# Performance work log

Measured on AMD Instinct MI355X. Metric: run time of the kernel, lower is better.

Reference implementation:

```python
import jax, jax.numpy as jnp
import numpy as np

OBJ_DIM, REL_DIM, EFF_DIM = 5, 1, 100
REL_HID, OBJ_HID, OUT_DIM = 150, 100, 2


def _init_linear(key, fan_in, fan_out):
    kw, kb = jax.random.split(key)
    bound = 1.0 / np.sqrt(fan_in)
    W = jax.random.uniform(kw, (fan_in, fan_out), jnp.float32, -bound, bound)
    b = jax.random.uniform(kb, (fan_out,), jnp.float32, -bound, bound)
    return W, b


def setup_inputs() -> dict:
    key = jax.random.key(0)
    ks = jax.random.split(key, 12)
    B, N, R = 64, 100, 9900
    inp = {
        "objects": jax.random.normal(ks[0], (B, N, OBJ_DIM), jnp.float32),
        "sender_relations": jax.random.uniform(ks[1], (B, N, R), jnp.float32),
        "receiver_relations": jax.random.uniform(ks[2], (B, N, R), jnp.float32),
        "relation_info": jax.random.normal(ks[3], (B, R, REL_DIM), jnp.float32),
    }
    # relational MLP: (2*obj + rel) -> 150 -> 150 -> effect_dim, ReLU after each
    rW1, rb1 = _init_linear(ks[4], 2 * OBJ_DIM + REL_DIM, REL_HID)
    rW2, rb2 = _init_linear(ks[5], REL_HID, REL_HID)
    rW3, rb3 = _init_linear(ks[6], REL_HID, EFF_DIM)
    # object MLP: (obj + effect) -> 100 -> 100 -> 2
    oW1, ob1 = _init_linear(ks[7], OBJ_DIM + EFF_DIM, OBJ_HID)
    oW2, ob2 = _init_linear(ks[8], OBJ_HID, OBJ_HID)
    oW3, ob3 = _init_linear(ks[9], OBJ_HID, OUT_DIM)
    inp.update(rW1=rW1, rb1=rb1, rW2=rW2, rb2=rb2, rW3=rW3, rb3=rb3,
               oW1=oW1, ob1=ob1, oW2=oW2, ob2=ob2, oW3=oW3, ob3=ob3)
    return inp


def _relational_mlp(x, rW1, rb1, rW2, rb2, rW3, rb3):
    h = jax.nn.relu(x @ rW1 + rb1)
    h = jax.nn.relu(h @ rW2 + rb2)
    return jax.nn.relu(h @ rW3 + rb3)


def _object_mlp(x, oW1, ob1, oW2, ob2, oW3, ob3):
    h = jax.nn.relu(x @ oW1 + ob1)
    h = jax.nn.relu(h @ oW2 + ob2)
    return h @ oW3 + ob3


def reference(objects, sender_relations, receiver_relations, relation_info,
              rW1, rb1, rW2, rb2, rW3, rb3, oW1, ob1, oW2, ob2, oW3, ob3):
    # gather: [B,R,N] @ [B,N,D] -> [B,R,D]
    senders = jnp.einsum('bnr,bnd->brd', sender_relations, objects)
    receivers = jnp.einsum('bnr,bnd->brd', receiver_relations, objects)
    rel_in = jnp.concatenate([senders, receivers, relation_info], axis=2)
    effects = _relational_mlp(rel_in, rW1, rb1, rW2, rb2, rW3, rb3)  # [B,R,E]
    # scatter: [B,N,R] @ [B,R,E] -> [B,N,E]
    effect_receivers = jnp.einsum('bnr,bre->bne', receiver_relations, effects)
    obj_in = jnp.concatenate([objects, effect_receivers], axis=2)
    return _object_mlp(obj_in, oW1, ob1, oW2, ob2, oW3, ob3)  # [B,N,2]
```

## Files before the change

kernel.cpp:

```cpp
#include <hip/hip_runtime.h>
#include <hip/hip_bf16.h>

#define B_    64
#define N_    100
#define R_    9900
#define OBJD  5
#define EFF   100

typedef __bf16 bf16x8 __attribute__((ext_vector_type(8)));
typedef __bf16 bf16x2 __attribute__((ext_vector_type(2)));
typedef short  short8v __attribute__((ext_vector_type(8)));
typedef float  f32x4  __attribute__((ext_vector_type(4)));

__device__ __forceinline__ ushort f2bf(float f) {
    __bf16 h = (__bf16)f;
    return __builtin_bit_cast(ushort, h);
}
__device__ __forceinline__ unsigned pk2(float a, float b) {
    bf16x2 v; v[0] = (__bf16)a; v[1] = (__bf16)b;
    return __builtin_bit_cast(unsigned, v);
}
__device__ __forceinline__ float bf2f(ushort u) {
    union { unsigned u; float f; } x; x.u = ((unsigned)u) << 16;
    return x.f;
}

#define WTR_OBJ 52096

__global__ __launch_bounds__(256) void k_prepw(
    const float* __restrict__ W1, const float* __restrict__ W2,
    const float* __restrict__ W3, const float* __restrict__ O1,
    const float* __restrict__ O2, const float* __restrict__ O3,
    ushort* __restrict__ WTR)
{
    const int img = blockIdx.x;
    if (img == 0) {
        for (int idx = threadIdx.x; idx < 6400; idx += 256) {
            const int c = idx / 40, k = idx - (idx/40)*40;
            WTR[idx] = f2bf((c < 150 && k < 11) ? W1[k*150 + c] : 0.f);
        }
    } else if (img == 1) {
        for (int idx = threadIdx.x; idx < 26880; idx += 256) {
            const int c = idx / 168, k = idx - (idx/168)*168;
            WTR[6400 + idx] = f2bf((c < 150 && k < 150) ? W2[k*150 + c] : 0.f);
        }
    } else if (img == 2) {
        for (int idx = threadIdx.x; idx < 18816; idx += 256) {
            const int c = idx / 168, k = idx - (idx/168)*168;
            WTR[33280 + idx] = f2bf((c < 100 && k < 150) ? W3[k*100 + c] : 0.f);
        }
    } else {
        const int j = img - 3;
        ushort* dst = WTR + WTR_OBJ + (size_t)j*11520;
        for (int idx = threadIdx.x; idx < 11520; idx += 256) {
            const int cc = idx / 72, kk = idx - (idx/72)*72;
            float v = 0.f;
            if (kk < 64) {
                if (j < 4) {
                    const int kg = j*64 + kk;
                    int row = -1;
                    if (kg < 5) row = kg;
                    else if (kg >= 8 && kg < 108) row = kg - 3;
                    else if (kg >= 108 && kg < 208) row = kg - 103;
                    if (cc < 100 && row >= 0) v = O1[row*100 + cc];
                } else if (j < 6) {
                    const int kg = (j-4)*64 + kk;
                    if (cc < 100 && kg < 100) v = O2[kg*100 + cc];
                } else {
                    const int kg = (j-6)*64 + kk;
                    if (cc < 2 && kg < 100) v = O3[kg*2 + cc];
                }
            }
            dst[idx] = f2bf(v);
        }
    }
}

#define LW1 0
#define LW2 6400
#define LW3 33280
#define LBA 52096
#define LBB 60160
#define LACT 68224
#define LBIAS 78976
#define LGB  79776
#define LTOT 81312

__global__ __launch_bounds__(512, 1) void k_relmlp_p(
    const float* __restrict__ obj, const float* __restrict__ SR,
    const float* __restrict__ RR, const float* __restrict__ RI,
    const ushort* __restrict__ WTR,
    const float* __restrict__ b1, const float* __restrict__ b2,
    const float* __restrict__ b3, float* __restrict__ ER)
{
    __shared__ __align__(16) ushort lds[LTOT];
    const int t  = threadIdx.x;
    const int b  = blockIdx.x >> 2;
    const int qt = blockIdx.x & 3;
    const int lane = t & 63, w = t >> 6;
    const int lo = lane & 15, hi = lane >> 4;
    const int mt = w & 3, nh = w >> 2;
    const int q  = t & 7,  rr = t >> 3;

    #pragma unroll
    for (int j = 0; j < 13; ++j) {
        const int idx = t + j*512;
        if (idx < 6512)
            reinterpret_cast<uint4*>(lds)[idx] =
                reinterpret_cast<const uint4*>(WTR)[idx];
    }
    {
        float* bias_w = (float*)(lds + LBIAS);
        if (t < 150)      bias_w[t] = b1[t];
        else if (t < 300) bias_w[t] = b2[t-150];
        else if (t < 400) bias_w[t] = b3[t-300];
    }
    if (t < 216) {
        ushort* base = lds + ((t < 108) ? LBA : LBB) + 100*72;
        const int k = (t < 108) ? t : t - 108;
        *reinterpret_cast<uint4*>(base + k*8) = make_uint4(0u, 0u, 0u, 0u);
    }
    if (t < 64) {
        ushort* gb0 = lds + LGB + t*24;
        gb0[11] = 0;
        *reinterpret_cast<ushort4*>(&gb0[12]) = make_ushort4(0,0,0,0);
        *reinterpret_cast<ushort4*>(&gb0[16]) = make_ushort4(0,0,0,0);
        *reinterpret_cast<ushort4*>(&gb0[20]) = make_ushort4(0,0,0,0);
    }

    float objv[13][5];
    {
        const int n0 = q*13;
        #pragma unroll
        for (int i = 0; i < 13; ++i) {
            const int n = n0 + i;
            #pragma unroll
            for (int d = 0; d < 5; ++d)
                objv[i][d] = (n < N_) ? obj[(size_t)b*500 + n*5 + d] : 0.f;
        }
    }

    const int tile0 = qt*39;
    const int tile1 = (tile0 + 39 < 155) ? tile0 + 39 : 155;

    ushort* bufA = lds + LBA;
    ushort* bufB = lds + LBB;
    ushort* act  = lds + LACT;
    ushort* gb   = lds + LGB;
    const float* bias = (const float*)(lds + LBIAS);

    f32x4 acc_er[7];
    #pragma unroll
    for (int ct = 0; ct < 7; ++ct) acc_er[ct] = (f32x4){0.f, 0.f, 0.f, 0.f};

    float4 psr[4], prr[4];
    float pri = 0.f, pri_n = 0.f;
    auto load4 = [&](float4* p, const float* M, int tile) {
        const int rr0 = tile*64;
        const int nr = (R_ - rr0 < 64) ? R_ - rr0 : 64;
        #pragma unroll
        for (int i = 0; i < 4; ++i) {
            const int idx = t + i*512;
            const int ci = idx < 1600 ? idx : 1599;
            const int n = ci >> 4, qq = ci & 15;
            const int col = (qq*4 < nr) ? qq*4 : 0;
            p[i] = *reinterpret_cast<const float4*>(
                &M[((size_t)b*N_ + n)*R_ + rr0 + col]);
        }
    };
    auto store4 = [&](const float4* p, ushort* dst, int nrow) {
        #pragma unroll
        for (int i = 0; i < 4; ++i) {
            const int idx = t + i*512;
            if (idx < 1600) {
                const int n = idx >> 4, qq = idx & 15;
                float4 v = p[i];
                if (qq*4 >= nrow) v = make_float4(0.f, 0.f, 0.f, 0.f);
                uint2 u; u.x = pk2(v.x, v.y); u.y = pk2(v.z, v.w);
                *reinterpret_cast<uint2*>(&dst[n*72 + qq*4]) = u;
            }
        }
    };
    auto loadRI = [&](int tile) -> float {
        const int rr0 = tile*64;
        return (t < 64 && rr0 + t < R_) ? RI[(size_t)b*R_ + rr0 + t] : 0.f;
    };

    load4(psr, SR, tile0);
    load4(prr, RR, tile0);
    pri = loadRI(tile0);
    __syncthreads();

    for (int tile = tile0; tile < tile1; ++tile) {
        const int r0 = tile*64;
        const int nrow = (R_ - r0 < 64) ? R_ - r0 : 64;

        store4(psr, bufA, nrow);
        store4(prr, bufB, nrow);
        if (tile + 1 < tile1) {
            load4(psr, SR, tile+1);
            load4(prr, RR, tile+1);
            pri_n = loadRI(tile+1);
        }
        __syncthreads();

        {
            float s0=0.f,s1=0.f,s2=0.f,s3=0.f,s4=0.f;
            float g0=0.f,g1=0.f,g2=0.f,g3=0.f,g4=0.f;
            const int n0 = q*13;
            #pragma unroll
            for (int i = 0; i < 13; ++i) {
                const int n = n0 + i;
                const float ms = bf2f(bufA[n*72 + rr]);
                const float mr = bf2f(bufB[n*72 + rr]);
                s0 += ms*objv[i][0]; s1 += ms*objv[i][1]; s2 += ms*objv[i][2];
                s3 += ms*objv[i][3]; s4 += ms*objv[i][4];
                g0 += mr*objv[i][0]; g1 += mr*objv[i][1]; g2 += mr*objv[i][2];
                g3 += mr*objv[i][3]; g4 += mr*objv[i][4];
            }
            #pragma unroll
            for (int msk = 1; msk < 8; msk <<= 1) {
                s0 += __shfl_xor(s0, msk); s1 += __shfl_xor(s1, msk);
                s2 += __shfl_xor(s2, msk); s3 += __shfl_xor(s3, msk);
                s4 += __shfl_xor(s4, msk);
                g0 += __shfl_xor(g0, msk); g1 += __shfl_xor(g1, msk);
                g2 += __shfl_xor(g2, msk); g3 += __shfl_xor(g3, msk);
                g4 += __shfl_xor(g4, msk);
            }
            if (q < 5) {
                const float sv = (q==0)?s0:(q==1)?s1:(q==2)?s2:(q==3)?s3:s4;
                const float gv = (q==0)?g0:(q==1)?g1:(q==2)?g2:(q==3)?g3:g4;
                gb[rr*24 + q]     = f2bf(sv);
                gb[rr*24 + 5 + q] = f2bf(gv);
            }
            if (t < 64) gb[t*24 + 10] = f2bf(pri);
            pri = pri_n;
        }
        __syncthreads();

        {
            f32x4 acc[5];
            #pragma unroll
            for (int j = 0; j < 5; ++j) {
                const int c = (nh*5 + j)*16 + lo;
                const float bv = (c < 150) ? bias[c] : 0.f;
                acc[j][0]=bv; acc[j][1]=bv; acc[j][2]=bv; acc[j][3]=bv;
            }
            bf16x8 a = __builtin_bit_cast(bf16x8, (short8v)0);
            if (hi < 2)
                a = *reinterpret_cast<const bf16x8*>(
                    &gb[(mt*16 + lo)*24 + hi*8]);
            #pragma unroll
            for (int j = 0; j < 5; ++j) {
                const int ct = nh*5 + j;
                const bf16x8 bb = *reinterpret_cast<const bf16x8*>(
                    &lds[LW1 + (ct*16 + lo)*40 + hi*8]);
                acc[j] = __builtin_amdgcn_mfma_f32_16x16x32_bf16(a, bb, acc[j], 0,0,0);
            }
            #pragma unroll
            for (int j = 0; j < 5; ++j) {
                const int ct = nh*5 + j;
                #pragma unroll
                for (int r = 0; r < 4; ++r)
                    act[(mt*16 + hi*4 + r)*168 + ct*16 + lo] =
                        f2bf(fmaxf(acc[j][r], 0.f));
            }
            __syncthreads();
        }
        {
            f32x4 acc[5];
            #pragma unroll
            for (int j = 0; j < 5; ++j) {
                const int c = (nh*5 + j)*16 + lo;
                const float bv = (c < 150) ? bias[150 + c] : 0.f;
                acc[j][0]=bv; acc[j][1]=bv; acc[j][2]=bv; acc[j][3]=bv;
            }
            #pragma unroll
            for (int ks = 0; ks < 5; ++ks) {
                const bf16x8 a = *reinterpret_cast<const bf16x8*>(
                    &act[(mt*16 + lo)*168 + ks*32 + hi*8]);
                #pragma unroll
                for (int j = 0; j < 5; ++j) {
                    const int ct = nh*5 + j;
                    const bf16x8 bb = *reinterpret_cast<const bf16x8*>(
                        &lds[LW2 + (ct*16 + lo)*168 + ks*32 + hi*8]);
                    acc[j] = __builtin_amdgcn_mfma_f32_16x16x32_bf16(a, bb, acc[j], 0,0,0);
                }
            }
            __syncthreads();
            #pragma unroll
            for (int j = 0; j < 5; ++j) {
                const int ct = nh*5 + j;
                #pragma unroll
                for (int r = 0; r < 4; ++r)
                    act[(mt*16 + hi*4 + r)*168 + ct*16 + lo] =
                        f2bf(fmaxf(acc[j][r], 0.f));
            }
            __syncthreads();
        }
        {
            const int nct = nh ? 3 : 4;
            f32x4 acc[4];
            #pragma unroll
            for (int j = 0; j < 4; ++j) {
                const int c = (nh*4 + j)*16 + lo;
                const float bv = (c < 100) ? bias[300 + c] : 0.f;
                acc[j][0]=bv; acc[j][1]=bv; acc[j][2]=bv; acc[j][3]=bv;
            }
            #pragma unroll
            for (int ks = 0; ks < 5; ++ks) {
                const bf16x8 a = *reinterpret_cast<const bf16x8*>(
                    &act[(mt*16 + lo)*168 + ks*32 + hi*8]);
                #pragma unroll
                for (int j = 0; j < 4; ++j) {
                    if (j < nct) {
                        const int ct = nh*4 + j;
                        const bf16x8 bb = *reinterpret_cast<const bf16x8*>(
                            &lds[LW3 + (ct*16 + lo)*168 + ks*32 + hi*8]);
                        acc[j] = __builtin_amdgcn_mfma_f32_16x16x32_bf16(a, bb, acc[j], 0,0,0);
                    }
                }
            }
            #pragma unroll
            for (int j = 0; j < 4; ++j) {
                if (j < nct) {
                    const int e = (nh*4 + j)*16 + lo;
                    if (e < 100) {
                        uint2 u;
                        u.x = pk2(fmaxf(acc[j][0], 0.f), fmaxf(acc[j][1], 0.f));
                        u.y = pk2(fmaxf(acc[j][2], 0.f), fmaxf(acc[j][3], 0.f));
                        *reinterpret_cast<uint2*>(&bufA[e*72 + mt*16 + hi*4]) = u;
                    }
                }
            }
            __syncthreads();
        }

        if (w < 7) {
            #pragma unroll
            for (int ks = 0; ks < 2; ++ks) {
                const bf16x8 a = *reinterpret_cast<const bf16x8*>(
                    &bufB[(w*16 + lo)*72 + ks*32 + hi*8]);
                #pragma unroll
                for (int ct = 0; ct < 7; ++ct) {
                    const bf16x8 bb = *reinterpret_cast<const bf16x8*>(
                        &bufA[(ct*16 + lo)*72 + ks*32 + hi*8]);
                    acc_er[ct] = __builtin_amdgcn_mfma_f32_16x16x32_bf16(
                        a, bb, acc_er[ct], 0, 0, 0);
                }
            }
        }
        __syncthreads();
    }

    if (w < 7) {
        float* ERq = ER + ((size_t)qt*B_ + b)*(size_t)(N_*EFF);
        #pragma unroll
        for (int ct = 0; ct < 7; ++ct) {
            const int e = ct*16 + lo;
            if (e < EFF) {
                #pragma unroll
                for (int rg = 0; rg < 4; ++rg) {
                    const int n = w*16 + hi*4 + rg;
                    if (n < N_)
                        ERq[n*EFF + e] = acc_er[ct][rg];
                }
            }
        }
    }
}

__device__ __forceinline__ void img_load(const ushort* __restrict__ g,
                                         uint4* pre, int t) {
    #pragma unroll
    for (int j = 0; j < 6; ++j) {
        int idx = t + j*256;
        int cidx = idx < 1440 ? idx : 1439;
        pre[j] = *reinterpret_cast<const uint4*>(g + (size_t)cidx*8);
    }
}
__device__ __forceinline__ void img_store(const uint4* pre, ushort* wt, int t) {
    #pragma unroll
    for (int j = 0; j < 6; ++j) {
        int idx = t + j*256;
        if (idx < 1440)
            *reinterpret_cast<uint4*>(wt + (size_t)idx*8) = pre[j];
    }
}

template<int COUT, int NCHUNK, int LASTKS, int NCT, bool RELU, int EPI, int ASTR>
__device__ __forceinline__ void mfma_layerO(
    const ushort* __restrict__ WT, const float* __restrict__ Bias,
    ushort* act, ushort* wt, int t, float* gout, int grow0)
{
    const int lane = t & 63;
    const int wv   = t >> 6;
    const int lo   = lane & 15;
    const int hi   = lane >> 4;

    f32x4 acc[2][NCT];
    #pragma unroll
    for (int ct = 0; ct < NCT; ++ct) {
        const int c = ct*16 + lo;
        const float bv = (c < COUT) ? Bias[c] : 0.f;
        #pragma unroll
        for (int m = 0; m < 2; ++m) {
            acc[m][ct][0] = bv; acc[m][ct][1] = bv;
            acc[m][ct][2] = bv; acc[m][ct][3] = bv;
        }
    }

    uint4 pre[6];
    img_load(WT, pre, t);
    #pragma unroll
    for (int q = 0; q < NCHUNK; ++q) {
        __syncthreads();
        img_store(pre, wt, t);
        if (q + 1 < NCHUNK) img_load(WT + (size_t)(q+1)*11520, pre, t);
        __syncthreads();
        const int nks = (q == NCHUNK-1) ? LASTKS : 2;
        #pragma unroll
        for (int ks = 0; ks < 2; ++ks) {
            if (ks < nks) {
                const int kg = q*64 + ks*32;
                const bf16x8 a0 = *reinterpret_cast<const bf16x8*>(
                    &act[(wv*32 +      lo)*ASTR + kg + hi*8]);
                const bf16x8 a1 = *reinterpret_cast<const bf16x8*>(
                    &act[(wv*32 + 16 + lo)*ASTR + kg + hi*8]);
                #pragma unroll
                for (int ct = 0; ct < NCT; ++ct) {
                    const bf16x8 b = *reinterpret_cast<const bf16x8*>(
                        &wt[(ct*16 + lo)*72 + ks*32 + hi*8]);
                    acc[0][ct] = __builtin_amdgcn_mfma_f32_16x16x32_bf16(
                        a0, b, acc[0][ct], 0, 0, 0);
                    acc[1][ct] = __builtin_amdgcn_mfma_f32_16x16x32_bf16(
                        a1, b, acc[1][ct], 0, 0, 0);
                }
            }
        }
    }

    __syncthreads();
    if (EPI == 0) {
        #pragma unroll
        for (int m = 0; m < 2; ++m)
            #pragma unroll
            for (int ct = 0; ct < NCT; ++ct)
                #pragma unroll
                for (int r = 0; r < 4; ++r) {
                    float v = acc[m][ct][r];
                    if (RELU) v = fmaxf(v, 0.f);
                    act[(wv*32 + m*16 + hi*4 + r)*ASTR + ct*16 + lo] = f2bf(v);
                }
    } else {
        #pragma unroll
        for (int m = 0; m < 2; ++m)
            #pragma unroll
            for (int r = 0; r < 4; ++r)
                if (lo < 2)
                    gout[(size_t)(grow0 + wv*32 + m*16 + hi*4 + r)*2 + lo] =
                        acc[m][0][r];
    }
    __syncthreads();
}

#define OSTR 232
#define ERSL ((size_t)B_*N_*EFF)

__global__ __launch_bounds__(256, 1) void k_objmlp_mfma(
    const float* __restrict__ obj, const float* __restrict__ ER,
    const ushort* __restrict__ WO,
    const float* __restrict__ ob1, const float* __restrict__ ob2,
    const float* __restrict__ ob3, float* __restrict__ out)
{
    __shared__ __align__(16) ushort act[128*OSTR];
    __shared__ __align__(16) ushort wt[160*72];
    const int t = threadIdx.x;
    const int rowbase = blockIdx.x * 128;

    float4 per[13];
    #pragma unroll
    for (int j = 0; j < 13; ++j) {
        const int idx = t + j*256;
        const int ci = idx < 3200 ? idx : 3199;
        const int row = ci / 25, c = ci - row*25;
        const float* p = &ER[(size_t)(rowbase + row)*100 + c*4];
        const float4 a0 = *reinterpret_cast<const float4*>(p);
        const float4 a1 = *reinterpret_cast<const float4*>(p + ERSL);
        const float4 a2 = *reinterpret_cast<const float4*>(p + 2*ERSL);
        const float4 a3 = *reinterpret_cast<const float4*>(p + 3*ERSL);
        per[j] = make_float4(a0.x + a1.x + a2.x + a3.x,
                             a0.y + a1.y + a2.y + a3.y,
                             a0.z + a1.z + a2.z + a3.z,
                             a0.w + a1.w + a2.w + a3.w);
    }
    #pragma unroll
    for (int j = 0; j < 13; ++j) {
        const int idx = t + j*256;
        if (idx < 3200) {
            const int row = idx / 25, c = idx - row*25;
            ushort h[4], l[4];
            #pragma unroll
            for (int k = 0; k < 4; ++k) {
                const float f = ((const float*)&per[j])[k];
                h[k] = f2bf(f);
                l[k] = f2bf(f - bf2f(h[k]));
            }
            *reinterpret_cast<ushort4*>(&act[row*OSTR + 8 + c*4]) =
                make_ushort4(h[0], h[1], h[2], h[3]);
            *reinterpret_cast<ushort4*>(&act[row*OSTR + 108 + c*4]) =
                make_ushort4(l[0], l[1], l[2], l[3]);
        }
    }
    #pragma unroll
    for (int j = 0; j < 3; ++j) {
        const int idx = t + j*256;
        if (idx < 640) {
            const int row = idx / 5, d = idx - row*5;
            act[row*OSTR + d] = f2bf(obj[(size_t)(rowbase + row)*5 + d]);
        }
    }
    #pragma unroll
    for (int j = 0; j < 2; ++j) {
        const int idx = t + j*256;
        if (idx < 384) {
            const int row = idx / 3, c = 5 + (idx - row*3);
            act[row*OSTR + c] = 0;
        }
    }
    #pragma unroll
    for (int j = 0; j < 2; ++j) {
        const int idx = t + j*256;
        if (idx < 512) {
            const int row = idx >> 2, p = idx & 3;
            *reinterpret_cast<ushort4*>(&act[row*OSTR + 208 + p*4]) =
                make_ushort4(0, 0, 0, 0);
        }
    }

    mfma_layerO<100, 4, 1, 7, true,  0, OSTR>(WO,           ob1, act, wt, t, nullptr, 0);
    mfma_layerO<100, 2, 2, 7, true,  0, OSTR>(WO + 4*11520, ob2, act, wt, t, nullptr, 0);
    mfma_layerO<2,   2, 2, 1, false, 2, OSTR>(WO + 6*11520, ob3, act, wt, t, out, rowbase);
}

extern "C" void kernel_launch(void* const* d_in, const int* in_sizes, int n_in,
                              void* d_out, int out_size, void* d_ws, size_t ws_size,
                              hipStream_t stream)
{
    const float* objects = (const float*)d_in[0];
    const float* SR      = (const float*)d_in[1];
    const float* RR      = (const float*)d_in[2];
    const float* RI      = (const float*)d_in[3];
    const float* rW1 = (const float*)d_in[4];  const float* rb1 = (const float*)d_in[5];
    const float* rW2 = (const float*)d_in[6];  const float* rb2 = (const float*)d_in[7];
    const float* rW3 = (const float*)d_in[8];  const float* rb3 = (const float*)d_in[9];
    const float* oW1 = (const float*)d_in[10]; const float* ob1 = (const float*)d_in[11];
    const float* oW2 = (const float*)d_in[12]; const float* ob2 = (const float*)d_in[13];
    const float* oW3 = (const float*)d_in[14]; const float* ob3 = (const float*)d_in[15];
    float* out = (float*)d_out;

    char* ws = (char*)d_ws;
    float*  ERp = (float*)ws;
    ushort* WTR = (ushort*)(ws + (size_t)4*B_*N_*EFF*sizeof(float));

    k_prepw<<<dim3(11), 256, 0, stream>>>(rW1, rW2, rW3, oW1, oW2, oW3, WTR);

    k_relmlp_p<<<dim3(256), 512, 0, stream>>>(objects, SR, RR, RI, WTR,
                                              rb1, rb2, rb3, ERp);

    k_objmlp_mfma<<<dim3(50), 256, 0, stream>>>(objects, ERp, WTR + WTR_OBJ,
                                                ob1, ob2, ob3, out);
}
```

Baseline: 366.9 us.

## Stream W2/W3 fragments from global to shrink LDS and run 8 slices per batch

W2 and W3 weights are no longer staged in shared memory. They are pre-packed into an MFMA fragment layout in global memory and read directly per lane, which cuts LDS per block from about 160KB to about 70KB and allows several blocks per CU (launch bounds now 512,4). The relation dimension is split into 8 slices per batch instead of 4, giving 512 blocks, and the object MLP now sums 8 partial ER slices. The trade-off is more global/L2 traffic for weight reads on every tile, plus a larger partial-sum buffer to write and reduce.

```diff
diff --git a/kernel.cpp b/kernel.cpp
--- a/kernel.cpp
+++ b/kernel.cpp
@@ -9,7 +9,6 @@
 
 typedef __bf16 bf16x8 __attribute__((ext_vector_type(8)));
 typedef __bf16 bf16x2 __attribute__((ext_vector_type(2)));
-typedef short  short8v __attribute__((ext_vector_type(8)));
 typedef float  f32x4  __attribute__((ext_vector_type(4)));
 
 __device__ __forceinline__ ushort f2bf(float f) {
@@ -26,6 +25,8 @@
 }
 
 #define WTR_OBJ 52096
+#define W2F_OFF 144256
+#define W3F_OFF 169856
 
 __global__ __launch_bounds__(256) void k_prepw(
     const float* __restrict__ W1, const float* __restrict__ W2,
@@ -48,6 +49,24 @@
         for (int idx = threadIdx.x; idx < 18816; idx += 256) {
             const int c = idx / 168, k = idx - (idx/168)*168;
             WTR[33280 + idx] = f2bf((c < 100 && k < 150) ? W3[k*100 + c] : 0.f);
+        }
+    } else if (img == 11) {
+        for (int idx = threadIdx.x; idx < 25600; idx += 256) {
+            const int ctks = idx >> 9;
+            const int ct = ctks / 5, ks = ctks - ct*5;
+            const int lane = (idx >> 3) & 63, e = idx & 7;
+            const int c = ct*16 + (lane & 15);
+            const int k = ks*32 + (lane >> 4)*8 + e;
+            WTR[W2F_OFF + idx] = f2bf((c < 150 && k < 150) ? W2[k*150 + c] : 0.f);
+        }
+    } else if (img == 12) {
+        for (int idx = threadIdx.x; idx < 17920; idx += 256) {
+            const int ctks = idx >> 9;
+            const int ct = ctks / 5, ks = ctks - ct*5;
+            const int lane = (idx >> 3) & 63, e = idx & 7;
+            const int c = ct*16 + (lane & 15);
+            const int k = ks*32 + (lane >> 4)*8 + e;
+            WTR[W3F_OFF + idx] = f2bf((c < 100 && k < 150) ? W3[k*100 + c] : 0.f);
         }
     } else {
         const int j = img - 3;
@@ -76,17 +95,15 @@
     }
 }
 
-#define LW1 0
-#define LW2 6400
-#define LW3 33280
-#define LBA 52096
-#define LBB 60160
-#define LACT 68224
-#define LBIAS 78976
-#define LGB  79776
-#define LTOT 81312
-
-__global__ __launch_bounds__(512, 1) void k_relmlp_p(
+#define LW1   0
+#define LBA   6400
+#define LBB   14464
+#define LACT  22528
+#define LBIAS 33280
+#define LGB   34080
+#define LTOT  35616
+
+__global__ __launch_bounds__(512, 4) void k_relmlp_p(
     const float* __restrict__ obj, const float* __restrict__ SR,
     const float* __restrict__ RR, const float* __restrict__ RI,
     const ushort* __restrict__ WTR,
@@ -94,18 +111,24 @@
     const float* __restrict__ b3, float* __restrict__ ER)
 {
     __shared__ __align__(16) ushort lds[LTOT];
-    const int t  = threadIdx.x;
-    const int b  = blockIdx.x >> 2;
-    const int qt = blockIdx.x & 3;
+    const int t   = threadIdx.x;
+    const int b   = blockIdx.x >> 3;
+    const int oct = blockIdx.x & 7;
     const int lane = t & 63, w = t >> 6;
     const int lo = lane & 15, hi = lane >> 4;
     const int mt = w & 3, nh = w >> 2;
     const int q  = t & 7,  rr = t >> 3;
 
-    #pragma unroll
-    for (int j = 0; j < 13; ++j) {
+    ushort* bufA = lds + LBA;
+    ushort* bufB = lds + LBB;
+    ushort* act  = lds + LACT;
+    ushort* gb   = lds + LGB;
+    const float* bias = (const float*)(lds + LBIAS);
+
+    #pragma unroll
+    for (int j = 0; j < 2; ++j) {
         const int idx = t + j*512;
-        if (idx < 6512)
+        if (idx < 800)
             reinterpret_cast<uint4*>(lds)[idx] =
                 reinterpret_cast<const uint4*>(WTR)[idx];
     }
@@ -116,12 +139,12 @@
         else if (t < 400) bias_w[t] = b3[t-300];
     }
     if (t < 216) {
-        ushort* base = lds + ((t < 108) ? LBA : LBB) + 100*72;
+        ushort* base = ((t < 108) ? bufA : bufB) + 100*72;
         const int k = (t < 108) ? t : t - 108;
         *reinterpret_cast<uint4*>(base + k*8) = make_uint4(0u, 0u, 0u, 0u);
     }
     if (t < 64) {
-        ushort* gb0 = lds + LGB + t*24;
+        ushort* gb0 = gb + t*24;
         gb0[11] = 0;
         *reinterpret_cast<ushort4*>(&gb0[12]) = make_ushort4(0,0,0,0);
         *reinterpret_cast<ushort4*>(&gb0[16]) = make_ushort4(0,0,0,0);
@@ -140,14 +163,8 @@
         }
     }
 
-    const int tile0 = qt*39;
-    const int tile1 = (tile0 + 39 < 155) ? tile0 + 39 : 155;
-
-    ushort* bufA = lds + LBA;
-    ushort* bufB = lds + LBB;
-    ushort* act  = lds + LACT;
-    ushort* gb   = lds + LGB;
-    const float* bias = (const float*)(lds + LBIAS);
+    const int tile0 = (oct*155) >> 3;
+    const int tile1 = ((oct+1)*155) >> 3;
 
     f32x4 acc_er[7];
     #pragma unroll
@@ -246,7 +263,7 @@
                 const float bv = (c < 150) ? bias[c] : 0.f;
                 acc[j][0]=bv; acc[j][1]=bv; acc[j][2]=bv; acc[j][3]=bv;
             }
-            bf16x8 a = __builtin_bit_cast(bf16x8, (short8v)0);
+            bf16x8 a = {};
             if (hi < 2)
                 a = *reinterpret_cast<const bf16x8*>(
                     &gb[(mt*16 + lo)*24 + hi*8]);
@@ -268,6 +285,8 @@
             __syncthreads();
         }
         {
+            const ushort* w2p = WTR + W2F_OFF + (size_t)lane*8 + (size_t)nh*12800;
+            asm volatile("" : "+v"(w2p));
             f32x4 acc[5];
             #pragma unroll
             for (int j = 0; j < 5; ++j) {
@@ -279,13 +298,16 @@
             for (int ks = 0; ks < 5; ++ks) {
                 const bf16x8 a = *reinterpret_cast<const bf16x8*>(
                     &act[(mt*16 + lo)*168 + ks*32 + hi*8]);
-                #pragma unroll
-                for (int j = 0; j < 5; ++j) {
-                    const int ct = nh*5 + j;
-                    const bf16x8 bb = *reinterpret_cast<const bf16x8*>(
-                        &lds[LW2 + (ct*16 + lo)*168 + ks*32 + hi*8]);
-                    acc[j] = __builtin_amdgcn_mfma_f32_16x16x32_bf16(a, bb, acc[j], 0,0,0);
-                }
+                const bf16x8 b0  = *reinterpret_cast<const bf16x8*>(w2p + ((0*5 + ks) << 9));
+                const bf16x8 b1v = *reinterpret_cast<const bf16x8*>(w2p + ((1*5 + ks) << 9));
+                const bf16x8 b2v = *reinterpret_cast<const bf16x8*>(w2p + ((2*5 + ks) << 9));
+                const bf16x8 b3v = *reinterpret_cast<const bf16x8*>(w2p + ((3*5 + ks) << 9));
+                const bf16x8 b4v = *reinterpret_cast<const bf16x8*>(w2p + ((4*5 + ks) << 9));
+                acc[0] = __builtin_amdgcn_mfma_f32_16x16x32_bf16(a, b0,  acc[0], 0,0,0);
+                acc[1] = __builtin_amdgcn_mfma_f32_16x16x32_bf16(a, b1v, acc[1], 0,0,0);
+                acc[2] = __builtin_amdgcn_mfma_f32_16x16x32_bf16(a, b2v, acc[2], 0,0,0);
+                acc[3] = __builtin_amdgcn_mfma_f32_16x16x32_bf16(a, b3v, acc[3], 0,0,0);
+                acc[4] = __builtin_amdgcn_mfma_f32_16x16x32_bf16(a, b4v, acc[4], 0,0,0);
             }
             __syncthreads();
             #pragma unroll
@@ -299,6 +321,8 @@
             __syncthreads();
         }
         {
+            const ushort* w3p = WTR + W3F_OFF + (size_t)lane*8 + (size_t)nh*10240;
+            asm volatile("" : "+v"(w3p));
             const int nct = nh ? 3 : 4;
             f32x4 acc[4];
             #pragma unroll
@@ -314,9 +338,8 @@
                 #pragma unroll
                 for (int j = 0; j < 4; ++j) {
                     if (j < nct) {
-                        const int ct = nh*4 + j;
                         const bf16x8 bb = *reinterpret_cast<const bf16x8*>(
-                            &lds[LW3 + (ct*16 + lo)*168 + ks*32 + hi*8]);
+                            w3p + ((j*5 + ks) << 9));
                         acc[j] = __builtin_amdgcn_mfma_f32_16x16x32_bf16(a, bb, acc[j], 0,0,0);
                     }
                 }
@@ -354,7 +377,7 @@
     }
 
     if (w < 7) {
-        float* ERq = ER + ((size_t)qt*B_ + b)*(size_t)(N_*EFF);
+        float* ERq = ER + ((size_t)oct*B_ + b)*(size_t)(N_*EFF);
         #pragma unroll
         for (int ct = 0; ct < 7; ++ct) {
             const int e = ct*16 + lo;
@@ -485,14 +508,13 @@
         const int ci = idx < 3200 ? idx : 3199;
         const int row = ci / 25, c = ci - row*25;
         const float* p = &ER[(size_t)(rowbase + row)*100 + c*4];
-        const float4 a0 = *reinterpret_cast<const float4*>(p);
-        const float4 a1 = *reinterpret_cast<const float4*>(p + ERSL);
-        const float4 a2 = *reinterpret_cast<const float4*>(p + 2*ERSL);
-        const float4 a3 = *reinterpret_cast<const float4*>(p + 3*ERSL);
-        per[j] = make_float4(a0.x + a1.x + a2.x + a3.x,
-                             a0.y + a1.y + a2.y + a3.y,
-                             a0.z + a1.z + a2.z + a3.z,
-                             a0.w + a1.w + a2.w + a3.w);
+        float4 s = make_float4(0.f, 0.f, 0.f, 0.f);
+        #pragma unroll
+        for (int sl = 0; sl < 8; ++sl) {
+            const float4 a = *reinterpret_cast<const float4*>(p + (size_t)sl*ERSL);
+            s.x += a.x; s.y += a.y; s.z += a.z; s.w += a.w;
+        }
+        per[j] = s;
     }
     #pragma unroll
     for (int j = 0; j < 13; ++j) {
@@ -561,11 +583,11 @@
 
     char* ws = (char*)d_ws;
     float*  ERp = (float*)ws;
-    ushort* WTR = (ushort*)(ws + (size_t)4*B_*N_*EFF*sizeof(float));
-
-    k_prepw<<<dim3(11), 256, 0, stream>>>(rW1, rW2, rW3, oW1, oW2, oW3, WTR);
-
-    k_relmlp_p<<<dim3(256), 512, 0, stream>>>(objects, SR, RR, RI, WTR,
+    ushort* WTR = (ushort*)(ws + (size_t)8*B_*N_*EFF*sizeof(float));
+
+    k_prepw<<<dim3(13), 256, 0, stream>>>(rW1, rW2, rW3, oW1, oW2, oW3, WTR);
+
+    k_relmlp_p<<<dim3(512), 512, 0, stream>>>(objects, SR, RR, RI, WTR,
                                               rb1, rb2, rb3, ERp);
 
     k_objmlp_mfma<<<dim3(50), 256, 0, stream>>>(objects, ERp, WTR + WTR_OBJ,
```

New measurement: 1.253 ms. 242% more time.
